# Kernel tuning notes

Measured on AMD Instinct MI355X. Metric: run time of the kernel, lower is better.

## Reference

```python
import jax, jax.numpy as jnp
import numpy as np

HEADS, DH = 8, 32

def _ln(x):
    m = x.mean(-1, keepdims=True)
    v = ((x - m) ** 2).mean(-1, keepdims=True)
    return (x - m) * jax.lax.rsqrt(v + 1e-5)

def _attn(xq, xk, ei, ea, wq, wk, wv, we, wo):
    # one relation: q from dst-type nodes xq, k/v from src-type nodes xk
    Nd, Ns, E = xq.shape[0], xk.shape[0], ea.shape[0]
    src, dst = ei[0], ei[1]
    q = (xq @ wq).reshape(Nd, HEADS, DH)
    k = (xk @ wk).reshape(Ns, HEADS, DH)
    v = (xk @ wv).reshape(Ns, HEADS, DH)
    e = (ea @ we).reshape(E, HEADS, DH)
    s = jnp.sum(q[dst] * (k[src] + e), axis=-1) * (DH ** -0.5)  # (E, heads)
    m = jax.ops.segment_max(s, dst, num_segments=Nd)
    m = jnp.where(jnp.isfinite(m), m, 0.0)
    ex = jnp.exp(s - m[dst])
    den = jax.ops.segment_sum(ex, dst, num_segments=Nd)
    msg = jax.ops.segment_sum(ex[:, :, None] * (v[src] + e), dst, num_segments=Nd)
    msg = msg / (den[:, :, None] + 1e-9)
    return msg.reshape(Nd, HEADS * DH) @ wo

def setup_inputs() -> dict:
    key = jax.random.key(0)
    ks = list(jax.random.split(key, 24))
    N, H, ED, L, F = 18432, 256, 64, 2, 512
    EA, ES = 294912, 65536
    nrm = lambda k, shp, s=1.0: jax.random.normal(k, shp, dtype=jnp.float32) * s
    inp = {}
    inp['all_feats_left'] = nrm(ks[0], (N, H))
    inp['all_feats_right'] = nrm(ks[1], (N, H))
    inp['ea_ll'] = nrm(ks[2], (EA, ED))
    inp['ea_rr'] = nrm(ks[3], (EA, ED))
    inp['ea_lr'] = nrm(ks[4], (ES, ED))
    inp['ea_rl'] = nrm(ks[5], (ES, ED))
    inp['ei_ll'] = jax.random.randint(ks[6], (2, EA), 0, N, dtype=jnp.int32)
    inp['ei_rr'] = jax.random.randint(ks[7], (2, EA), 0, N, dtype=jnp.int32)
    inp['ei_lr'] = jax.random.randint(ks[8], (2, ES), 0, N, dtype=jnp.int32)
    inp['ei_rl'] = jax.random.randint(ks[9], (2, ES), 0, N, dtype=jnp.int32)
    # relation order: 0=ll, 1=rr, 2=lr (src left -> dst right), 3=rl
    inp['Wq'] = nrm(ks[10], (L, 4, H, H), H ** -0.5)
    inp['Wk'] = nrm(ks[11], (L, 4, H, H), H ** -0.5)
    inp['Wv'] = nrm(ks[12], (L, 4, H, H), H ** -0.5)
    inp['We'] = nrm(ks[13], (L, 4, ED, H), ED ** -0.5)
    inp['Wo'] = nrm(ks[14], (L, 4, H, H), H ** -0.5)
    inp['ffn_w1'] = nrm(ks[15], (L, 2, H, F), H ** -0.5)
    inp['ffn_b1'] = jnp.zeros((L, 2, F), jnp.float32)
    inp['ffn_w2'] = nrm(ks[16], (L, 2, F, H), F ** -0.5)
    inp['ffn_b2'] = jnp.zeros((L, 2, H), jnp.float32)
    inp['head_w1'] = nrm(ks[17], (H, H), H ** -0.5)
    inp['head_b1'] = jnp.zeros((H,), jnp.float32)
    inp['head_w2'] = nrm(ks[18], (H, 7), H ** -0.5)
    inp['head_b2'] = jnp.zeros((7,), jnp.float32)
    inp['action_start'] = 2048  # slice(K, None), K current nodes per arm
    return inp

def reference(all_feats_left, all_feats_right, ea_ll, ea_rr, ea_lr, ea_rl,
              Wq, Wk, Wv, We, Wo, ffn_w1, ffn_b1, ffn_w2, ffn_b2,
              head_w1, head_b1, head_w2, head_b2,
              ei_ll, ei_rr, ei_lr, ei_rl, action_start):
    xl, xr = all_feats_left, all_feats_right
    L = Wq.shape[0]
    for l in range(L):
        agg_l = (_attn(xl, xl, ei_ll, ea_ll, Wq[l, 0], Wk[l, 0], Wv[l, 0], We[l, 0], Wo[l, 0])
                 + _attn(xl, xr, ei_rl, ea_rl, Wq[l, 3], Wk[l, 3], Wv[l, 3], We[l, 3], Wo[l, 3]))
        agg_r = (_attn(xr, xr, ei_rr, ea_rr, Wq[l, 1], Wk[l, 1], Wv[l, 1], We[l, 1], Wo[l, 1])
                 + _attn(xr, xl, ei_lr, ea_lr, Wq[l, 2], Wk[l, 2], Wv[l, 2], We[l, 2], Wo[l, 2]))
        xl = _ln(xl + agg_l)
        xr = _ln(xr + agg_r)
        xl = _ln(xl + jax.nn.gelu(xl @ ffn_w1[l, 0] + ffn_b1[l, 0]) @ ffn_w2[l, 0] + ffn_b2[l, 0])
        xr = _ln(xr + jax.nn.gelu(xr @ ffn_w1[l, 1] + ffn_b1[l, 1]) @ ffn_w2[l, 1] + ffn_b2[l, 1])
    la = xl[action_start:]
    ra = xr[action_start:]
    head = lambda z: jax.nn.gelu(z @ head_w1 + head_b1) @ head_w2 + head_b2
    return head(la), head(ra)
```

## Files before the change

### kernel.cpp

```cpp
#include <hip/hip_runtime.h>
#include <math.h>

typedef __attribute__((ext_vector_type(8))) short short8;
typedef __attribute__((ext_vector_type(4))) float f32x4;

__device__ __forceinline__ unsigned short f2bf(float f) {
  unsigned u = __builtin_bit_cast(unsigned, f);
  u += 0x7fff + ((u >> 16) & 1);
  return (unsigned short)(u >> 16);
}
__device__ __forceinline__ float bf2f(unsigned short h) {
  unsigned u = ((unsigned)h) << 16;
  return __builtin_bit_cast(float, u);
}
__device__ __forceinline__ float gelu_f(float x) {
  const float c0 = 0.7978845608028654f;
  return 0.5f * x * (1.0f + tanhf(c0 * (x + 0.044715f * x * x * x)));
}
__device__ __forceinline__ void gload16(const unsigned short* g, unsigned short* l) {
  __builtin_amdgcn_global_load_lds(
      (const __attribute__((address_space(1))) unsigned int*)g,
      (__attribute__((address_space(3))) unsigned int*)l, 16, 0, 0);
}

template<bool ACC, bool BIAS, bool GELU>
__global__ __launch_bounds__(256)
void gemm_mfma2_k(const unsigned short* __restrict__ A0, const unsigned short* __restrict__ A1,
                  int lda,
                  const unsigned short* __restrict__ BT0, const unsigned short* __restrict__ BT1,
                  const float* __restrict__ bias0, const float* __restrict__ bias1,
                  float* __restrict__ Cf0, float* __restrict__ Cf1, int Sf, int ldf,
                  unsigned short* __restrict__ Cb10, unsigned short* __restrict__ Cb11,
                  int S2, int ldb1,
                  unsigned short* __restrict__ Cb20, unsigned short* __restrict__ Cb21, int ldb2,
                  int M, int N, int K)
{
  const int z = blockIdx.z;
  const unsigned short* A  = z ? A1  : A0;
  const unsigned short* BT = z ? BT1 : BT0;
  const float* bias        = z ? bias1 : bias0;
  float* Cf                = z ? Cf1 : Cf0;
  unsigned short* Cb1      = z ? Cb11 : Cb10;
  unsigned short* Cb2      = z ? Cb21 : Cb20;

  __shared__ __align__(16) unsigned short As[128 * 32];
  __shared__ __align__(16) unsigned short Bs[128 * 32];
  const int tid = threadIdx.x;
  const int bm = blockIdx.x * 128, bn = blockIdx.y * 128;
  const int lane = tid & 63, w = tid >> 6;
  const int wr = w >> 1, wc = w & 1;
  const int l15 = lane & 15, kg = lane >> 4;

  const int srow0 = w * 16 + (lane >> 2);
  const int srow1 = 64 + srow0;
  const int sslot = lane & 3;
  const int koff0 = (((sslot - (srow0 >> 1)) & 3)) * 8;
  const int koff1 = (((sslot - (srow1 >> 1)) & 3)) * 8;
  const unsigned short* gA0 = A + (size_t)(bm + srow0) * lda + koff0;
  const unsigned short* gA1 = A + (size_t)(bm + srow1) * lda + koff1;
  const unsigned short* gB0 = BT + (size_t)(bn + srow0) * K + koff0;
  const unsigned short* gB1 = BT + (size_t)(bn + srow1) * K + koff1;
  unsigned short* lA0 = As + w * 512;
  unsigned short* lA1 = As + 2048 + w * 512;
  unsigned short* lB0 = Bs + w * 512;
  unsigned short* lB1 = Bs + 2048 + w * 512;

  f32x4 acc[4][4] = {};

  for (int k0 = 0; k0 < K; k0 += 32) {
    gload16(gA0 + k0, lA0);
    gload16(gA1 + k0, lA1);
    gload16(gB0 + k0, lB0);
    gload16(gB1 + k0, lB1);
    __syncthreads();
    short8 af[4], bfr[4];
#pragma unroll
    for (int m = 0; m < 4; ++m) {
      int row = wr * 64 + m * 16 + l15;
      int ph = (kg + (row >> 1)) & 3;
      af[m] = *(const short8*)(As + row * 32 + ph * 8);
    }
#pragma unroll
    for (int n = 0; n < 4; ++n) {
      int col = wc * 64 + n * 16 + l15;
      int ph = (kg + (col >> 1)) & 3;
      bfr[n] = *(const short8*)(Bs + col * 32 + ph * 8);
    }
#pragma unroll
    for (int m = 0; m < 4; ++m)
#pragma unroll
      for (int n = 0; n < 4; ++n)
        acc[m][n] = __builtin_amdgcn_mfma_f32_16x16x32_bf16(af[m], bfr[n], acc[m][n], 0, 0, 0);
    __syncthreads();
  }

#pragma unroll
  for (int m = 0; m < 4; ++m) {
#pragma unroll
    for (int n = 0; n < 4; ++n) {
      int col = bn + wc * 64 + n * 16 + l15;
      float bv = BIAS ? bias[col] : 0.f;
      f32x4 v = acc[m][n];
#pragma unroll
      for (int r2 = 0; r2 < 4; ++r2) {
        int row = bm + wr * 64 + m * 16 + kg * 4 + r2;
        float val = v[r2] + bv;
        if (GELU) val = gelu_f(val);
        if (col < Sf) {
          float* p = Cf + (size_t)row * ldf + col;
          if (ACC) val += *p;
          *p = val;
        } else if (col < S2) {
          Cb1[(size_t)row * ldb1 + (col - Sf)] = f2bf(val);
        } else {
          Cb2[(size_t)row * ldb2 + (col - S2)] = f2bf(val);
        }
      }
    }
  }
}

template<bool BIAS>
__global__ __launch_bounds__(256)
void gemm_k2(const float* __restrict__ A0, const float* __restrict__ A1,
             const float* __restrict__ B, const float* __restrict__ bias,
             float* __restrict__ C0, float* __restrict__ C1,
             int M, int N, int K)
{
  const float* A = blockIdx.z ? A1 : A0;
  float* C = blockIdx.z ? C1 : C0;
  __shared__ float As[16][132];
  __shared__ float Bs[16][132];
  const int tid = threadIdx.x;
  const int tx = tid & 15, ty = tid >> 4;
  const int bm = blockIdx.x * 128;
  float acc[8][8];
#pragma unroll
  for (int i = 0; i < 8; ++i)
#pragma unroll
    for (int j = 0; j < 8; ++j) acc[i][j] = 0.f;
  const int ar = tid >> 1;
  const int ac = (tid & 1) * 8;
  const int br = tid >> 4;
  const int bc = (tid & 15) * 8;
  for (int k0 = 0; k0 < K; k0 += 16) {
    {
      float av[8] = {0,0,0,0,0,0,0,0};
      if (bm + ar < M) {
        const float* app = A + (size_t)(bm + ar) * K + (k0 + ac);
        float4 a0 = *(const float4*)app;
        float4 a1 = *(const float4*)(app + 4);
        av[0]=a0.x; av[1]=a0.y; av[2]=a0.z; av[3]=a0.w;
        av[4]=a1.x; av[5]=a1.y; av[6]=a1.z; av[7]=a1.w;
      }
#pragma unroll
      for (int i = 0; i < 8; ++i) As[ac + i][ar] = av[i];
    }
    {
      float bv[8] = {0,0,0,0,0,0,0,0};
      const float* bpp = B + (size_t)(k0 + br) * N + bc;
#pragma unroll
      for (int i = 0; i < 8; ++i) { if (bc + i < N) bv[i] = bpp[i]; }
#pragma unroll
      for (int i = 0; i < 8; ++i) Bs[br][bc + i] = bv[i];
    }
    __syncthreads();
#pragma unroll
    for (int kk = 0; kk < 16; ++kk) {
      float a[8], b[8];
      float4 t0 = *(const float4*)&As[kk][ty * 8];
      float4 t1 = *(const float4*)&As[kk][ty * 8 + 4];
      float4 u0 = *(const float4*)&Bs[kk][tx * 8];
      float4 u1 = *(const float4*)&Bs[kk][tx * 8 + 4];
      a[0]=t0.x;a[1]=t0.y;a[2]=t0.z;a[3]=t0.w;a[4]=t1.x;a[5]=t1.y;a[6]=t1.z;a[7]=t1.w;
      b[0]=u0.x;b[1]=u0.y;b[2]=u0.z;b[3]=u0.w;b[4]=u1.x;b[5]=u1.y;b[6]=u1.z;b[7]=u1.w;
#pragma unroll
      for (int i = 0; i < 8; ++i)
#pragma unroll
        for (int j = 0; j < 8; ++j)
          acc[i][j] = fmaf(a[i], b[j], acc[i][j]);
    }
    __syncthreads();
  }
#pragma unroll
  for (int i = 0; i < 8; ++i) {
    int row = bm + ty * 8 + i;
    if (row >= M) continue;
    int colg = tx * 8;
    float* cp = C + (size_t)row * N + colg;
#pragma unroll
    for (int j = 0; j < 8; ++j) {
      int cc = colg + j;
      if (cc < N) {
        float val = acc[i][j];
        if (BIAS) val += bias[cc];
        cp[j] = val;
      }
    }
  }
}

__global__ void tc_k(const float* __restrict__ in, unsigned short* __restrict__ out,
                     int K, int N, int inStride, int outStride, int rowOff, int totK, int kOff)
{
  const int mat = blockIdx.y;
  const int idx = blockIdx.x * 256 + threadIdx.x;
  if (idx >= N * K) return;
  const int n = idx / K, k = idx - n * K;
  out[(size_t)mat * outStride + (size_t)(rowOff + n) * totK + kOff + k] =
      f2bf(in[(size_t)mat * inStride + (size_t)k * N + n]);
}

__global__ __launch_bounds__(256)
void wqe_k(unsigned short* __restrict__ BT, const float* __restrict__ We, int matStride)
{
  const int mat = blockIdx.y;
  const int oc = blockIdx.x;
  const int g = oc >> 6, cc = oc & 63;
  const int kin = threadIdx.x;
  const float* wrow = We + (size_t)mat * 16384 + (size_t)cc * 256 + g * 32;
  const unsigned short* bq = BT + (size_t)mat * matStride + (size_t)(g * 32) * 256 + kin;
  float acc = 0.f;
#pragma unroll 8
  for (int d = 0; d < 32; ++d)
    acc += bf2f(bq[(size_t)d * 256]) * wrow[d];
  BT[(size_t)mat * matStride + (size_t)(256 + oc) * 256 + kin] = f2bf(acc);
}

__global__ __launch_bounds__(256)
void wc_k(const float* __restrict__ We, const float* __restrict__ Wo,
          unsigned short* __restrict__ BTwo)
{
  const int mat = blockIdx.y;
  const int j = blockIdx.x;
  const int h = j >> 6, c = j & 63;
  const int n = threadIdx.x;
  const float* wep = We + (size_t)mat * 16384 + (size_t)c * 256 + h * 32;
  const float* wop = Wo + (size_t)mat * 65536 + (size_t)(h * 32) * 256 + n;
  float acc = 0.f;
#pragma unroll 8
  for (int d = 0; d < 32; ++d)
    acc += wep[d] * wop[(size_t)d * 256];
  BTwo[(size_t)mat * 196608 + (size_t)n * 768 + 256 + j] = f2bf(acc);
}

template<bool EABF>
__global__ __launch_bounds__(256)
void edge_attn_k(const int* __restrict__ offs, const int2* __restrict__ pairs,
                 const void* __restrict__ eaP, unsigned short* qTmsg,
                 const unsigned short* __restrict__ kv, int Nn)
{
  const int wv = (blockIdx.x * blockDim.x + threadIdx.x) >> 6;
  if (wv >= Nn) return;
  const int lane = threadIdx.x & 63;
  const int g = lane >> 3, p = lane & 7;
  const float scale = 0.17677669529663687f;
  const ushort4 qu = *(const ushort4*)(qTmsg + (size_t)wv * 768 + lane * 4);
  const float qx = bf2f(qu.x), qy = bf2f(qu.y), qz = bf2f(qu.z), qw = bf2f(qu.w);
  const unsigned short* Tp = qTmsg + (size_t)wv * 768 + 256 + g * 64 + p * 8;
  const ushort4 tu0 = *(const ushort4*)Tp;
  const ushort4 tu1 = *(const ushort4*)(Tp + 4);
  const float Ta0 = bf2f(tu0.x), Ta1 = bf2f(tu0.y), Ta2 = bf2f(tu0.z), Ta3 = bf2f(tu0.w);
  const float Tc0 = bf2f(tu1.x), Tc1 = bf2f(tu1.y), Tc2 = bf2f(tu1.z), Tc3 = bf2f(tu1.w);
  float m = -INFINITY, den = 0.f;
  float ax = 0.f, ay = 0.f, az = 0.f, aw = 0.f;
  float G[8] = {0,0,0,0,0,0,0,0};
  const int e0 = __builtin_amdgcn_readfirstlane(offs[wv]);
  const int e1 = __builtin_amdgcn_readfirstlane(offs[wv + 1]);
  for (int j = e0; j < e1; j += 2) {
    const bool hasB = (j + 1) < e1;
    const int2 prA = pairs[j];
    const int2 prB = hasB ? pairs[j + 1] : prA;
    float eA[8], eB[8];
    if (EABF) {
      const unsigned short* ebp = (const unsigned short*)eaP;
      const short8 eAu = *(const short8*)(ebp + (size_t)prA.x * 64 + p * 8);
      const short8 eBu = *(const short8*)(ebp + (size_t)prB.x * 64 + p * 8);
#pragma unroll
      for (int i = 0; i < 8; ++i) {
        eA[i] = bf2f((unsigned short)eAu[i]);
        eB[i] = bf2f((unsigned short)eBu[i]);
      }
    } else {
      const float* efp = (const float*)eaP;
      const float4 a0 = *(const float4*)(efp + (size_t)prA.x * 64 + p * 8);
      const float4 a1 = *(const float4*)(efp + (size_t)prA.x * 64 + p * 8 + 4);
      const float4 b0 = *(const float4*)(efp + (size_t)prB.x * 64 + p * 8);
      const float4 b1 = *(const float4*)(efp + (size_t)prB.x * 64 + p * 8 + 4);
      eA[0]=a0.x; eA[1]=a0.y; eA[2]=a0.z; eA[3]=a0.w;
      eA[4]=a1.x; eA[5]=a1.y; eA[6]=a1.z; eA[7]=a1.w;
      eB[0]=b0.x; eB[1]=b0.y; eB[2]=b0.z; eB[3]=b0.w;
      eB[4]=b1.x; eB[5]=b1.y; eB[6]=b1.z; eB[7]=b1.w;
    }
    const unsigned short* kpA = kv + (size_t)prA.y * 512 + lane * 4;
    const unsigned short* kpB = kv + (size_t)prB.y * 512 + lane * 4;
    const ushort4 kAu = *(const ushort4*)kpA;
    const ushort4 vAu = *(const ushort4*)(kpA + 256);
    const ushort4 kBu = *(const ushort4*)kpB;
    const ushort4 vBu = *(const ushort4*)(kpB + 256);
    float pA = qx * bf2f(kAu.x) + qy * bf2f(kAu.y) + qz * bf2f(kAu.z) + qw * bf2f(kAu.w);
    pA += eA[0]*Ta0 + eA[1]*Ta1 + eA[2]*Ta2 + eA[3]*Ta3;
    pA += eA[4]*Tc0 + eA[5]*Tc1 + eA[6]*Tc2 + eA[7]*Tc3;
    float pB = qx * bf2f(kBu.x) + qy * bf2f(kBu.y) + qz * bf2f(kBu.z) + qw * bf2f(kBu.w);
    pB += eB[0]*Ta0 + eB[1]*Ta1 + eB[2]*Ta2 + eB[3]*Ta3;
    pB += eB[4]*Tc0 + eB[5]*Tc1 + eB[6]*Tc2 + eB[7]*Tc3;
    pA += __shfl_xor(pA, 1, 64); pA += __shfl_xor(pA, 2, 64); pA += __shfl_xor(pA, 4, 64);
    pB += __shfl_xor(pB, 1, 64); pB += __shfl_xor(pB, 2, 64); pB += __shfl_xor(pB, 4, 64);
    const float sA = pA * scale;
    const float sB = hasB ? pB * scale : -INFINITY;
    const float mn = fmaxf(m, fmaxf(sA, sB));
    const float corr = __expf(m - mn);
    const float wA = __expf(sA - mn);
    const float wB = __expf(sB - mn);
    m = mn;
    den = den * corr + wA + wB;
    ax = ax * corr + wA * bf2f(vAu.x) + wB * bf2f(vBu.x);
    ay = ay * corr + wA * bf2f(vAu.y) + wB * bf2f(vBu.y);
    az = az * corr + wA * bf2f(vAu.z) + wB * bf2f(vBu.z);
    aw = aw * corr + wA * bf2f(vAu.w) + wB * bf2f(vBu.w);
#pragma unroll
    for (int i = 0; i < 8; ++i)
      G[i] = G[i] * corr + wA * eA[i] + wB * eB[i];
  }
  const float inv = 1.f / (den + 1e-9f);
  ushort4 o;
  o.x = f2bf(ax * inv); o.y = f2bf(ay * inv);
  o.z = f2bf(az * inv); o.w = f2bf(aw * inv);
  *(ushort4*)(qTmsg + (size_t)wv * 768 + lane * 4) = o;
  short8 gn;
#pragma unroll
  for (int i = 0; i < 8; ++i) gn[i] = (short)f2bf(G[i] * inv);
  *(short8*)(qTmsg + (size_t)wv * 768 + 256 + g * 64 + p * 8) = gn;
}

__global__ __launch_bounds__(256)
void add_ln2_k(unsigned short* __restrict__ xbL, const float* __restrict__ addL,
               unsigned short* __restrict__ xbR, const float* __restrict__ addR, int Nn)
{
  unsigned short* xb = blockIdx.y ? xbR : xbL;
  const float* add = blockIdx.y ? addR : addL;
  const int wv = (blockIdx.x * blockDim.x + threadIdx.x) >> 6;
  if (wv >= Nn) return;
  const int lane = threadIdx.x & 63;
  ushort4 xu = *(const ushort4*)(xb + (size_t)wv * 256 + lane * 4);
  float4 av = *(const float4*)(add + (size_t)wv * 256 + lane * 4);
  float4 y;
  y.x = bf2f(xu.x) + av.x; y.y = bf2f(xu.y) + av.y;
  y.z = bf2f(xu.z) + av.z; y.w = bf2f(xu.w) + av.w;
  float s = y.x + y.y + y.z + y.w;
#pragma unroll
  for (int msk = 1; msk < 64; msk <<= 1) s += __shfl_xor(s, msk, 64);
  const float mean = s * (1.f / 256.f);
  float4 d;
  d.x = y.x - mean; d.y = y.y - mean; d.z = y.z - mean; d.w = y.w - mean;
  float sq = d.x*d.x + d.y*d.y + d.z*d.z + d.w*d.w;
#pragma unroll
  for (int msk = 1; msk < 64; msk <<= 1) sq += __shfl_xor(sq, msk, 64);
  const float r = rsqrtf(sq * (1.f / 256.f) + 1e-5f);
  ushort4 ob;
  ob.x = f2bf(d.x * r); ob.y = f2bf(d.y * r);
  ob.z = f2bf(d.z * r); ob.w = f2bf(d.w * r);
  *(ushort4*)(xb + (size_t)wv * 256 + lane * 4) = ob;
}

__global__ void cvt_x2_k(const float* __restrict__ aL, unsigned short* __restrict__ xbL,
                         const float* __restrict__ aR, unsigned short* __restrict__ xbR, int n4)
{
  const float* a = blockIdx.y ? aR : aL;
  unsigned short* xb = blockIdx.y ? xbR : xbL;
  int i = blockIdx.x * 256 + threadIdx.x;
  if (i >= n4) return;
  float4 v = ((const float4*)a)[i];
  ushort4 b;
  b.x = f2bf(v.x); b.y = f2bf(v.y); b.z = f2bf(v.z); b.w = f2bf(v.w);
  ((ushort4*)xb)[i] = b;
}

__global__ void cvt_ea2_k(const float* __restrict__ s0, const float* __restrict__ s1,
                          unsigned short* __restrict__ d0, unsigned short* __restrict__ d1,
                          int n8a, int n8b)
{
  const float* src = blockIdx.y ? s1 : s0;
  unsigned short* dst = blockIdx.y ? d1 : d0;
  const int n8 = blockIdx.y ? n8b : n8a;
  int i = blockIdx.x * 256 + threadIdx.x;
  if (i >= n8) return;
  float4 a = ((const float4*)src)[i * 2];
  float4 b = ((const float4*)src)[i * 2 + 1];
  short8 o;
  o[0] = (short)f2bf(a.x); o[1] = (short)f2bf(a.y);
  o[2] = (short)f2bf(a.z); o[3] = (short)f2bf(a.w);
  o[4] = (short)f2bf(b.x); o[5] = (short)f2bf(b.y);
  o[6] = (short)f2bf(b.z); o[7] = (short)f2bf(b.w);
  *(short8*)(dst + (size_t)i * 8) = o;
}

__global__ void zero4_k(int* p, int n) {
  int i = blockIdx.x * 256 + threadIdx.x;
  if (i < n) p[i] = 0;
}
__global__ void hist4_k(const int* d0, const int* d1, const int* d2, const int* d3,
                        int E0, int E1, int E2, int E3, int* cnt, int Nn) {
  const int s = blockIdx.y;
  const int* d = (s == 0) ? d0 : (s == 1) ? d1 : (s == 2) ? d2 : d3;
  const int E = (s == 0) ? E0 : (s == 1) ? E1 : (s == 2) ? E2 : E3;
  int e = blockIdx.x * 256 + threadIdx.x;
  if (e < E) atomicAdd(&cnt[s * Nn + d[e]], 1);
}
__global__ __launch_bounds__(256)
void scan4_k(const int* __restrict__ cnt, int* __restrict__ offs, int* __restrict__ cursor, int Nn)
{
  __shared__ int sums[256];
  const int s = blockIdx.x;
  const int t = threadIdx.x;
  const int* c = cnt + (size_t)s * Nn;
  int* o = offs + (size_t)s * (Nn + 1);
  int* cur = cursor + (size_t)s * Nn;
  const int chunk = (Nn + 255) / 256;
  const int base = t * chunk;
  int sl = 0;
  for (int i = 0; i < chunk; ++i) {
    int idx = base + i;
    if (idx < Nn) sl += c[idx];
  }
  sums[t] = sl;
  __syncthreads();
  for (int off = 1; off < 256; off <<= 1) {
    int val = (t >= off) ? sums[t - off] : 0;
    __syncthreads();
    sums[t] += val;
    __syncthreads();
  }
  int run = (t == 0) ? 0 : sums[t - 1];
  for (int i = 0; i < chunk; ++i) {
    int idx = base + i;
    if (idx < Nn) { o[idx] = run; cur[idx] = run; run += c[idx]; }
  }
  if (t == 255) o[Nn] = run;
}
__global__ void scatter4_k(const int* e0p, const int* e1p, const int* e2p, const int* e3p,
                           int E0, int E1, int E2, int E3, int* cursor,
                           int2* p0, int2* p1, int2* p2, int2* p3, int Nn) {
  const int s = blockIdx.y;
  const int* ei = (s == 0) ? e0p : (s == 1) ? e1p : (s == 2) ? e2p : e3p;
  int2* po = (s == 0) ? p0 : (s == 1) ? p1 : (s == 2) ? p2 : p3;
  const int E = (s == 0) ? E0 : (s == 1) ? E1 : (s == 2) ? E2 : E3;
  int e = blockIdx.x * 256 + threadIdx.x;
  if (e < E) {
    int pos = atomicAdd(&cursor[s * Nn + ei[E + e]], 1);
    po[pos] = make_int2(e, ei[e]);
  }
}

extern "C" void kernel_launch(void* const* d_in, const int* in_sizes, int n_in,
                              void* d_out, int out_size, void* d_ws, size_t ws_size,
                              hipStream_t stream)
{
  (void)n_in; (void)ws_size;
  const float* afl = (const float*)d_in[0];
  const float* afr = (const float*)d_in[1];
  const float* eaA[4] = {(const float*)d_in[2], (const float*)d_in[3],
                         (const float*)d_in[4], (const float*)d_in[5]};
  const int* eiA[4] = {(const int*)d_in[6], (const int*)d_in[7],
                       (const int*)d_in[8], (const int*)d_in[9]};
  const float* Wq  = (const float*)d_in[10];
  const float* Wk  = (const float*)d_in[11];
  const float* Wv  = (const float*)d_in[12];
  const float* We  = (const float*)d_in[13];
  const float* Wo  = (const float*)d_in[14];
  const float* fw1 = (const float*)d_in[15];
  const float* fb1 = (const float*)d_in[16];
  const float* fw2 = (const float*)d_in[17];
  const float* fb2 = (const float*)d_in[18];
  const float* hw1 = (const float*)d_in[19];
  const float* hb1 = (const float*)d_in[20];
  const float* hw2 = (const float*)d_in[21];
  const float* hb2 = (const float*)d_in[22];

  const int Nn = in_sizes[0] / 256;
  const int E[4] = {in_sizes[2] / 64, in_sizes[3] / 64, in_sizes[4] / 64, in_sizes[5] / 64};
  const int Mh = out_size / 14;
  const int astart = Nn - Mh;
  float* out = (float*)d_out;

  char* wsp = (char*)d_ws;
  auto alloc = [&](size_t bytes) -> void* {
    void* pp = (void*)wsp;
    wsp += (bytes + 255) & ~(size_t)255;
    return pp;
  };
  unsigned short* xlb = (unsigned short*)alloc((size_t)Nn * 256 * 2);
  unsigned short* xrb = (unsigned short*)alloc((size_t)Nn * 256 * 2);
  float* aggL = (float*)alloc((size_t)Nn * 256 * 4);
  float* aggR = (float*)alloc((size_t)Nn * 256 * 4);
  unsigned short* qTbA = (unsigned short*)alloc((size_t)Nn * 768 * 2);
  unsigned short* qTbB = (unsigned short*)alloc((size_t)Nn * 768 * 2);
  unsigned short* kvbA = (unsigned short*)alloc((size_t)Nn * 512 * 2);
  unsigned short* kvbB = (unsigned short*)alloc((size_t)Nn * 512 * 2);
  unsigned short* BTqkvT = (unsigned short*)alloc((size_t)8 * 1280 * 256 * 2);
  unsigned short* BTwo   = (unsigned short*)alloc((size_t)8 * 256 * 768 * 2);
  unsigned short* BTf1   = (unsigned short*)alloc((size_t)4 * 512 * 256 * 2);
  unsigned short* BTf2   = (unsigned short*)alloc((size_t)4 * 256 * 512 * 2);
  unsigned short* BTh1   = (unsigned short*)alloc((size_t)256 * 256 * 2);
  unsigned short* eabf0  = (unsigned short*)alloc((size_t)E[0] * 64 * 2);
  unsigned short* eabf1  = (unsigned short*)alloc((size_t)E[1] * 64 * 2);
  int* offs4 = (int*)alloc((size_t)4 * (Nn + 1) * 4);
  int* cnt4  = (int*)alloc((size_t)4 * Nn * 4);
  int* cur4  = (int*)alloc((size_t)4 * Nn * 4);
  int2* pairs[4];
  for (int s = 0; s < 4; ++s) pairs[s] = (int2*)alloc((size_t)E[s] * 8);

  const dim3 B256(256);
  const int wgNodes = (Nn * 64 + 255) / 256;
  int maxE = E[0];
  for (int s = 1; s < 4; ++s) if (E[s] > maxE) maxE = E[s];

  cvt_x2_k<<<dim3((Nn * 64 + 255) / 256, 2), B256, 0, stream>>>(afl, xlb, afr, xrb, Nn * 64);
  {
    int n8a = E[0] * 8, n8b = E[1] * 8;
    int gx = ((n8a > n8b ? n8a : n8b) + 255) / 256;
    cvt_ea2_k<<<dim3(gx, 2), B256, 0, stream>>>(eaA[0], eaA[1], eabf0, eabf1, n8a, n8b);
  }
  zero4_k<<<dim3((4 * Nn + 255) / 256), B256, 0, stream>>>(cnt4, 4 * Nn);
  {
    dim3 gh((maxE + 255) / 256, 4);
    hist4_k<<<gh, B256, 0, stream>>>(eiA[0] + E[0], eiA[1] + E[1], eiA[2] + E[2], eiA[3] + E[3],
                                     E[0], E[1], E[2], E[3], cnt4, Nn);
    scan4_k<<<dim3(4), B256, 0, stream>>>(cnt4, offs4, cur4, Nn);
    scatter4_k<<<gh, B256, 0, stream>>>(eiA[0], eiA[1], eiA[2], eiA[3],
                                        E[0], E[1], E[2], E[3], cur4,
                                        pairs[0], pairs[1], pairs[2], pairs[3], Nn);
  }
  {
    dim3 g8((65536 + 255) / 256, 8);
    tc_k<<<g8, B256, 0, stream>>>(Wq, BTqkvT, 256, 256, 65536, 327680, 0,    256, 0);
    tc_k<<<g8, B256, 0, stream>>>(Wk, BTqkvT, 256, 256, 65536, 327680, 768,  256, 0);
    tc_k<<<g8, B256, 0, stream>>>(Wv, BTqkvT, 256, 256, 65536, 327680, 1024, 256, 0);
    wqe_k<<<dim3(512, 8), B256, 0, stream>>>(BTqkvT, We, 327680);
    tc_k<<<g8, B256, 0, stream>>>(Wo, BTwo, 256, 256, 65536, 196608, 0, 768, 0);
    wc_k<<<dim3(512, 8), B256, 0, stream>>>(We, Wo, BTwo);
    tc_k<<<dim3((131072 + 255) / 256, 4), B256, 0, stream>>>(fw1, BTf1, 256, 512, 131072, 131072, 0, 256, 0);
    tc_k<<<dim3((131072 + 255) / 256, 4), B256, 0, stream>>>(fw2, BTf2, 512, 256, 131072, 131072, 0, 512, 0);
    tc_k<<<dim3((65536 + 255) / 256, 1), B256, 0, stream>>>(hw1, BTh1, 256, 256, 0, 0, 0, 256, 0);
  }

  auto mfma2 = [&](const unsigned short* A0, const unsigned short* A1, int lda,
                   const unsigned short* BT0, const unsigned short* BT1,
                   const float* bias0, const float* bias1,
                   float* Cf0, float* Cf1, int Sf, int ldf,
                   unsigned short* Cb10, unsigned short* Cb11, int S2, int ldb1,
                   unsigned short* Cb20, unsigned short* Cb21, int ldb2,
                   int M, int N, int K, bool accf, bool biasf, bool gelu) {
    dim3 g(M / 128, N / 128, 2);
    if (accf)
      gemm_mfma2_k<true, false, false><<<g, B256, 0, stream>>>(A0, A1, lda, BT0, BT1, bias0, bias1,
          Cf0, Cf1, Sf, ldf, Cb10, Cb11, S2, ldb1, Cb20, Cb21, ldb2, M, N, K);
    else if (biasf && gelu)
      gemm_mfma2_k<false, true, true ><<<g, B256, 0, stream>>>(A0, A1, lda, BT0, BT1, bias0, bias1,
          Cf0, Cf1, Sf, ldf, Cb10, Cb11, S2, ldb1, Cb20, Cb21, ldb2, M, N, K);
    else if (biasf)
      gemm_mfma2_k<false, true, false><<<g, B256, 0, stream>>>(A0, A1, lda, BT0, BT1, bias0, bias1,
          Cf0, Cf1, Sf, ldf, Cb10, Cb11, S2, ldb1, Cb20, Cb21, ldb2, M, N, K);
    else
      gemm_mfma2_k<false, false, false><<<g, B256, 0, stream>>>(A0, A1, lda, BT0, BT1, bias0, bias1,
          Cf0, Cf1, Sf, ldf, Cb10, Cb11, S2, ldb1, Cb20, Cb21, ldb2, M, N, K);
  };
  auto edge = [&](int s, unsigned short* qTmsg, const unsigned short* kvb) {
    if (s <= 1) {
      const unsigned short* eb = s == 0 ? eabf0 : eabf1;
      edge_attn_k<true><<<dim3(wgNodes), B256, 0, stream>>>(
          offs4 + (size_t)s * (Nn + 1), pairs[s], (const void*)eb, qTmsg, kvb, Nn);
    } else {
      edge_attn_k<false><<<dim3(wgNodes), B256, 0, stream>>>(
          offs4 + (size_t)s * (Nn + 1), pairs[s], (const void*)eaA[s], qTmsg, kvb, Nn);
    }
  };

  for (int l = 0; l < 2; ++l) {
    const unsigned short* btLL = BTqkvT + (size_t)(l*4+0) * 327680;
    const unsigned short* btRR = BTqkvT + (size_t)(l*4+1) * 327680;
    const unsigned short* btLR = BTqkvT + (size_t)(l*4+2) * 327680;
    const unsigned short* btRL = BTqkvT + (size_t)(l*4+3) * 327680;
    mfma2(xlb, xrb, 256, btLL, btRR, nullptr, nullptr, nullptr, nullptr, 0, 0,
          qTbA, qTbB, 768, 768, kvbA, kvbB, 512, Nn, 1280, 256, false, false, false);
    edge(0, qTbA, kvbA);
    edge(1, qTbB, kvbB);
    mfma2(qTbA, qTbB, 768, BTwo + (size_t)(l*4+0)*196608, BTwo + (size_t)(l*4+1)*196608,
          nullptr, nullptr, aggL, aggR, 256, 256, nullptr, nullptr, 0, 0, nullptr, nullptr, 0,
          Nn, 256, 768, false, false, false);
    mfma2(xlb, xrb, 256, btRL, btLR, nullptr, nullptr, nullptr, nullptr, 0, 0,
          qTbA, qTbB, 768, 768, nullptr, nullptr, 0, Nn, 768, 256, false, false, false);
    mfma2(xrb, xlb, 256, btRL + (size_t)768 * 256, btLR + (size_t)768 * 256,
          nullptr, nullptr, nullptr, nullptr, 0, 0,
          nullptr, nullptr, 0, 0, kvbA, kvbB, 512, Nn, 512, 256, false, false, false);
    edge(3, qTbA, kvbA);
    edge(2, qTbB, kvbB);
    mfma2(qTbA, qTbB, 768, BTwo + (size_t)(l*4+3)*196608, BTwo + (size_t)(l*4+2)*196608,
          nullptr, nullptr, aggL, aggR, 256, 256, nullptr, nullptr, 0, 0, nullptr, nullptr, 0,
          Nn, 256, 768, true, false, false);
    add_ln2_k<<<dim3(wgNodes, 2), B256, 0, stream>>>(xlb, aggL, xrb, aggR, Nn);
    const int fL = l * 2 + 0, fR = l * 2 + 1;
    mfma2(xlb, xrb, 256, BTf1 + (size_t)fL*131072, BTf1 + (size_t)fR*131072,
          fb1 + (size_t)fL*512, fb1 + (size_t)fR*512, nullptr, nullptr, 0, 0,
          nullptr, nullptr, 0, 0, kvbA, kvbB, 512, Nn, 512, 256, false, true, true);
    mfma2(kvbA, kvbB, 512, BTf2 + (size_t)fL*131072, BTf2 + (size_t)fR*131072,
          fb2 + (size_t)fL*256, fb2 + (size_t)fR*256, aggL, aggR, 256, 256,
          nullptr, nullptr, 0, 0, nullptr, nullptr, 0, Nn, 256, 512, false, true, false);
    add_ln2_k<<<dim3(wgNodes, 2), B256, 0, stream>>>(xlb, aggL, xrb, aggR, Nn);
  }
  mfma2(xlb + (size_t)astart * 256, xrb + (size_t)astart * 256, 256, BTh1, BTh1,
        hb1, hb1, aggL, aggR, 256, 256, nullptr, nullptr, 0, 0, nullptr, nullptr, 0,
        Mh, 256, 256, false, true, true);
  gemm_k2<true><<<dim3(Mh / 128, 1, 2), B256, 0, stream>>>(aggL, aggR, hw2, hb2,
                                                           out, out + (size_t)Mh * 7, Mh, 7, 256);
}
```

Before: 1.256 ms.

## Batch cross-relation projections and fuse both relations' output projections into one GEMM

```diff
diff --git a/kernel.cpp b/kernel.cpp
--- a/kernel.cpp
+++ b/kernel.cpp
@@ -23,7 +23,7 @@
       (__attribute__((address_space(3))) unsigned int*)l, 16, 0, 0);
 }
 
-template<bool ACC, bool BIAS, bool GELU>
+template<bool BIAS, bool GELU>
 __global__ __launch_bounds__(256)
 void gemm_mfma2_k(const unsigned short* __restrict__ A0, const unsigned short* __restrict__ A1,
                   int lda,
@@ -65,6 +65,18 @@
   unsigned short* lB0 = Bs + w * 512;
   unsigned short* lB1 = Bs + 2048 + w * 512;
 
+  int roffA[4], roffB[4];
+#pragma unroll
+  for (int m = 0; m < 4; ++m) {
+    int row = wr * 64 + m * 16 + l15;
+    roffA[m] = row * 32 + ((kg + (row >> 1)) & 3) * 8;
+  }
+#pragma unroll
+  for (int n = 0; n < 4; ++n) {
+    int col = wc * 64 + n * 16 + l15;
+    roffB[n] = col * 32 + ((kg + (col >> 1)) & 3) * 8;
+  }
+
   f32x4 acc[4][4] = {};
 
   for (int k0 = 0; k0 < K; k0 += 32) {
@@ -75,17 +87,9 @@
     __syncthreads();
     short8 af[4], bfr[4];
 #pragma unroll
-    for (int m = 0; m < 4; ++m) {
-      int row = wr * 64 + m * 16 + l15;
-      int ph = (kg + (row >> 1)) & 3;
-      af[m] = *(const short8*)(As + row * 32 + ph * 8);
-    }
-#pragma unroll
-    for (int n = 0; n < 4; ++n) {
-      int col = wc * 64 + n * 16 + l15;
-      int ph = (kg + (col >> 1)) & 3;
-      bfr[n] = *(const short8*)(Bs + col * 32 + ph * 8);
-    }
+    for (int m = 0; m < 4; ++m) af[m] = *(const short8*)(As + roffA[m]);
+#pragma unroll
+    for (int n = 0; n < 4; ++n) bfr[n] = *(const short8*)(Bs + roffB[n]);
 #pragma unroll
     for (int m = 0; m < 4; ++m)
 #pragma unroll
@@ -107,14 +111,97 @@
         float val = v[r2] + bv;
         if (GELU) val = gelu_f(val);
         if (col < Sf) {
-          float* p = Cf + (size_t)row * ldf + col;
-          if (ACC) val += *p;
-          *p = val;
+          Cf[(size_t)row * ldf + col] = val;
         } else if (col < S2) {
           Cb1[(size_t)row * ldb1 + (col - Sf)] = f2bf(val);
         } else {
           Cb2[(size_t)row * ldb2 + (col - S2)] = f2bf(val);
         }
+      }
+    }
+  }
+}
+
+__global__ __launch_bounds__(256)
+void gemm_mfma4_k(const unsigned short* __restrict__ Ax0, const unsigned short* __restrict__ Ax1,
+                  const unsigned short* __restrict__ Ax2, const unsigned short* __restrict__ Ax3,
+                  const unsigned short* __restrict__ Bx0, const unsigned short* __restrict__ Bx1,
+                  const unsigned short* __restrict__ Bx2, const unsigned short* __restrict__ Bx3,
+                  unsigned short* __restrict__ Cx0, unsigned short* __restrict__ Cx1,
+                  unsigned short* __restrict__ Cx2, unsigned short* __restrict__ Cx3,
+                  int ldb01, int ldb23, int N01, int N23, int lda, int K, int M)
+{
+  const int z = blockIdx.z;
+  const unsigned short* A; const unsigned short* BT; unsigned short* C;
+  int ldb, Nz;
+  if (z == 0)      { A = Ax0; BT = Bx0; C = Cx0; ldb = ldb01; Nz = N01; }
+  else if (z == 1) { A = Ax1; BT = Bx1; C = Cx1; ldb = ldb01; Nz = N01; }
+  else if (z == 2) { A = Ax2; BT = Bx2; C = Cx2; ldb = ldb23; Nz = N23; }
+  else             { A = Ax3; BT = Bx3; C = Cx3; ldb = ldb23; Nz = N23; }
+  const int bm = blockIdx.x * 128, bn = blockIdx.y * 128;
+  if (bn >= Nz) return;
+
+  __shared__ __align__(16) unsigned short As[128 * 32];
+  __shared__ __align__(16) unsigned short Bs[128 * 32];
+  const int tid = threadIdx.x;
+  const int lane = tid & 63, w = tid >> 6;
+  const int wr = w >> 1, wc = w & 1;
+  const int l15 = lane & 15, kg = lane >> 4;
+  const int srow0 = w * 16 + (lane >> 2);
+  const int srow1 = 64 + srow0;
+  const int sslot = lane & 3;
+  const int koff0 = (((sslot - (srow0 >> 1)) & 3)) * 8;
+  const int koff1 = (((sslot - (srow1 >> 1)) & 3)) * 8;
+  const unsigned short* gA0 = A + (size_t)(bm + srow0) * lda + koff0;
+  const unsigned short* gA1 = A + (size_t)(bm + srow1) * lda + koff1;
+  const unsigned short* gB0 = BT + (size_t)(bn + srow0) * K + koff0;
+  const unsigned short* gB1 = BT + (size_t)(bn + srow1) * K + koff1;
+  unsigned short* lA0 = As + w * 512;
+  unsigned short* lA1 = As + 2048 + w * 512;
+  unsigned short* lB0 = Bs + w * 512;
+  unsigned short* lB1 = Bs + 2048 + w * 512;
+
+  int roffA[4], roffB[4];
+#pragma unroll
+  for (int m = 0; m < 4; ++m) {
+    int row = wr * 64 + m * 16 + l15;
+    roffA[m] = row * 32 + ((kg + (row >> 1)) & 3) * 8;
+  }
+#pragma unroll
+  for (int n = 0; n < 4; ++n) {
+    int col = wc * 64 + n * 16 + l15;
+    roffB[n] = col * 32 + ((kg + (col >> 1)) & 3) * 8;
+  }
+
+  f32x4 acc[4][4] = {};
+  for (int k0 = 0; k0 < K; k0 += 32) {
+    gload16(gA0 + k0, lA0);
+    gload16(gA1 + k0, lA1);
+    gload16(gB0 + k0, lB0);
+    gload16(gB1 + k0, lB1);
+    __syncthreads();
+    short8 af[4], bfr[4];
+#pragma unroll
+    for (int m = 0; m < 4; ++m) af[m] = *(const short8*)(As + roffA[m]);
+#pragma unroll
+    for (int n = 0; n < 4; ++n) bfr[n] = *(const short8*)(Bs + roffB[n]);
+#pragma unroll
+    for (int m = 0; m < 4; ++m)
+#pragma unroll
+      for (int n = 0; n < 4; ++n)
+        acc[m][n] = __builtin_amdgcn_mfma_f32_16x16x32_bf16(af[m], bfr[n], acc[m][n], 0, 0, 0);
+    __syncthreads();
+  }
+#pragma unroll
+  for (int m = 0; m < 4; ++m) {
+#pragma unroll
+    for (int n = 0; n < 4; ++n) {
+      int col = bn + wc * 64 + n * 16 + l15;
+      f32x4 v = acc[m][n];
+#pragma unroll
+      for (int r2 = 0; r2 < 4; ++r2) {
+        int row = bm + wr * 64 + m * 16 + kg * 4 + r2;
+        C[(size_t)row * ldb + col] = f2bf(v[r2]);
       }
     }
   }
@@ -211,6 +298,19 @@
       f2bf(in[(size_t)mat * inStride + (size_t)k * N + n]);
 }
 
+__global__ void tc_qkv_k(const float* __restrict__ Wq, const float* __restrict__ Wk,
+                         const float* __restrict__ Wv, unsigned short* __restrict__ out)
+{
+  const int zz = blockIdx.z;
+  const float* in = (zz == 0) ? Wq : (zz == 1) ? Wk : Wv;
+  const int rowOff = (zz == 0) ? 0 : (zz == 1) ? 768 : 1024;
+  const int mat = blockIdx.y;
+  const int idx = blockIdx.x * 256 + threadIdx.x;
+  const int n = idx >> 8, k = idx & 255;
+  out[(size_t)mat * 327680 + (size_t)(rowOff + n) * 256 + k] =
+      f2bf(in[(size_t)mat * 65536 + (size_t)k * 256 + n]);
+}
+
 __global__ __launch_bounds__(256)
 void wqe_k(unsigned short* __restrict__ BT, const float* __restrict__ We, int matStride)
 {
@@ -227,9 +327,21 @@
   BT[(size_t)mat * matStride + (size_t)(256 + oc) * 256 + kin] = f2bf(acc);
 }
 
+__global__ void wo_tc_k(const float* __restrict__ Wo, unsigned short* __restrict__ BTwoF)
+{
+  const int mat = blockIdx.y;
+  const int idx = blockIdx.x * 256 + threadIdx.x;
+  const int n = idx >> 8, k = idx & 255;
+  const int l = mat >> 2, i = mat & 3;
+  const int side = (i == 1 || i == 2) ? 1 : 0;
+  const int base = (i >= 2) ? 768 : 0;
+  BTwoF[(size_t)(l * 2 + side) * 393216 + (size_t)n * 1536 + base + k] =
+      f2bf(Wo[(size_t)mat * 65536 + (size_t)k * 256 + n]);
+}
+
 __global__ __launch_bounds__(256)
 void wc_k(const float* __restrict__ We, const float* __restrict__ Wo,
-          unsigned short* __restrict__ BTwo)
+          unsigned short* __restrict__ BTwoF)
 {
   const int mat = blockIdx.y;
   const int j = blockIdx.x;
@@ -241,23 +353,35 @@
 #pragma unroll 8
   for (int d = 0; d < 32; ++d)
     acc += wep[d] * wop[(size_t)d * 256];
-  BTwo[(size_t)mat * 196608 + (size_t)n * 768 + 256 + j] = f2bf(acc);
+  const int l = mat >> 2, i = mat & 3;
+  const int side = (i == 1 || i == 2) ? 1 : 0;
+  const int base = (i >= 2) ? 768 : 0;
+  BTwoF[(size_t)(l * 2 + side) * 393216 + (size_t)n * 1536 + base + 256 + j] = f2bf(acc);
 }
 
 template<bool EABF>
 __global__ __launch_bounds__(256)
-void edge_attn_k(const int* __restrict__ offs, const int2* __restrict__ pairs,
-                 const void* __restrict__ eaP, unsigned short* qTmsg,
-                 const unsigned short* __restrict__ kv, int Nn)
-{
+void edge2_k(const int* __restrict__ o0, const int* __restrict__ o1,
+             const int2* __restrict__ p0, const int2* __restrict__ p1,
+             const void* __restrict__ e0, const void* __restrict__ e1,
+             unsigned short* q0, unsigned short* q1,
+             const unsigned short* __restrict__ k0, const unsigned short* __restrict__ k1,
+             int Nn)
+{
+  const int y = blockIdx.y;
+  const int* offs = y ? o1 : o0;
+  const int2* pairs = y ? p1 : p0;
+  const void* eaP = y ? e1 : e0;
+  unsigned short* qTmsg = y ? q1 : q0;
+  const unsigned short* kv = y ? k1 : k0;
   const int wv = (blockIdx.x * blockDim.x + threadIdx.x) >> 6;
   if (wv >= Nn) return;
   const int lane = threadIdx.x & 63;
   const int g = lane >> 3, p = lane & 7;
   const float scale = 0.17677669529663687f;
-  const ushort4 qu = *(const ushort4*)(qTmsg + (size_t)wv * 768 + lane * 4);
+  const ushort4 qu = *(const ushort4*)(qTmsg + (size_t)wv * 1536 + lane * 4);
   const float qx = bf2f(qu.x), qy = bf2f(qu.y), qz = bf2f(qu.z), qw = bf2f(qu.w);
-  const unsigned short* Tp = qTmsg + (size_t)wv * 768 + 256 + g * 64 + p * 8;
+  const unsigned short* Tp = qTmsg + (size_t)wv * 1536 + 256 + g * 64 + p * 8;
   const ushort4 tu0 = *(const ushort4*)Tp;
   const ushort4 tu1 = *(const ushort4*)(Tp + 4);
   const float Ta0 = bf2f(tu0.x), Ta1 = bf2f(tu0.y), Ta2 = bf2f(tu0.z), Ta3 = bf2f(tu0.w);
@@ -265,10 +389,10 @@
   float m = -INFINITY, den = 0.f;
   float ax = 0.f, ay = 0.f, az = 0.f, aw = 0.f;
   float G[8] = {0,0,0,0,0,0,0,0};
-  const int e0 = __builtin_amdgcn_readfirstlane(offs[wv]);
-  const int e1 = __builtin_amdgcn_readfirstlane(offs[wv + 1]);
-  for (int j = e0; j < e1; j += 2) {
-    const bool hasB = (j + 1) < e1;
+  const int e0i = __builtin_amdgcn_readfirstlane(offs[wv]);
+  const int e1i = __builtin_amdgcn_readfirstlane(offs[wv + 1]);
+  for (int j = e0i; j < e1i; j += 2) {
+    const bool hasB = (j + 1) < e1i;
     const int2 prA = pairs[j];
     const int2 prB = hasB ? pairs[j + 1] : prA;
     float eA[8], eB[8];
@@ -326,27 +450,27 @@
   ushort4 o;
   o.x = f2bf(ax * inv); o.y = f2bf(ay * inv);
   o.z = f2bf(az * inv); o.w = f2bf(aw * inv);
-  *(ushort4*)(qTmsg + (size_t)wv * 768 + lane * 4) = o;
+  *(ushort4*)(qTmsg + (size_t)wv * 1536 + lane * 4) = o;
   short8 gn;
 #pragma unroll
   for (int i = 0; i < 8; ++i) gn[i] = (short)f2bf(G[i] * inv);
-  *(short8*)(qTmsg + (size_t)wv * 768 + 256 + g * 64 + p * 8) = gn;
+  *(short8*)(qTmsg + (size_t)wv * 1536 + 256 + g * 64 + p * 8) = gn;
 }
 
 __global__ __launch_bounds__(256)
-void add_ln2_k(unsigned short* __restrict__ xbL, const float* __restrict__ addL,
-               unsigned short* __restrict__ xbR, const float* __restrict__ addR, int Nn)
+void add_ln2_k(unsigned short* __restrict__ xbL, const unsigned short* __restrict__ addL,
+               unsigned short* __restrict__ xbR, const unsigned short* __restrict__ addR, int Nn)
 {
   unsigned short* xb = blockIdx.y ? xbR : xbL;
-  const float* add = blockIdx.y ? addR : addL;
+  const unsigned short* add = blockIdx.y ? addR : addL;
   const int wv = (blockIdx.x * blockDim.x + threadIdx.x) >> 6;
   if (wv >= Nn) return;
   const int lane = threadIdx.x & 63;
   ushort4 xu = *(const ushort4*)(xb + (size_t)wv * 256 + lane * 4);
-  float4 av = *(const float4*)(add + (size_t)wv * 256 + lane * 4);
+  ushort4 au = *(const ushort4*)(add + (size_t)wv * 256 + lane * 4);
   float4 y;
-  y.x = bf2f(xu.x) + av.x; y.y = bf2f(xu.y) + av.y;
-  y.z = bf2f(xu.z) + av.z; y.w = bf2f(xu.w) + av.w;
+  y.x = bf2f(xu.x) + bf2f(au.x); y.y = bf2f(xu.y) + bf2f(au.y);
+  y.z = bf2f(xu.z) + bf2f(au.z); y.w = bf2f(xu.w) + bf2f(au.w);
   float s = y.x + y.y + y.z + y.w;
 #pragma unroll
   for (int msk = 1; msk < 64; msk <<= 1) s += __shfl_xor(s, msk, 64);
@@ -376,13 +500,8 @@
   ((ushort4*)xb)[i] = b;
 }
 
-__global__ void cvt_ea2_k(const float* __restrict__ s0, const float* __restrict__ s1,
-                          unsigned short* __restrict__ d0, unsigned short* __restrict__ d1,
-                          int n8a, int n8b)
-{
-  const float* src = blockIdx.y ? s1 : s0;
-  unsigned short* dst = blockIdx.y ? d1 : d0;
-  const int n8 = blockIdx.y ? n8b : n8a;
+__global__ void cvt_ea1_k(const float* __restrict__ src, unsigned short* __restrict__ dst, int n8)
+{
   int i = blockIdx.x * 256 + threadIdx.x;
   if (i >= n8) return;
   float4 a = ((const float4*)src)[i * 2];
@@ -491,19 +610,18 @@
   };
   unsigned short* xlb = (unsigned short*)alloc((size_t)Nn * 256 * 2);
   unsigned short* xrb = (unsigned short*)alloc((size_t)Nn * 256 * 2);
-  float* aggL = (float*)alloc((size_t)Nn * 256 * 4);
-  float* aggR = (float*)alloc((size_t)Nn * 256 * 4);
-  unsigned short* qTbA = (unsigned short*)alloc((size_t)Nn * 768 * 2);
-  unsigned short* qTbB = (unsigned short*)alloc((size_t)Nn * 768 * 2);
+  unsigned short* aggLb = (unsigned short*)alloc((size_t)Nn * 256 * 2);
+  unsigned short* aggRb = (unsigned short*)alloc((size_t)Nn * 256 * 2);
+  unsigned short* qTmsgA = (unsigned short*)alloc((size_t)Nn * 1536 * 2);
+  unsigned short* qTmsgB = (unsigned short*)alloc((size_t)Nn * 1536 * 2);
   unsigned short* kvbA = (unsigned short*)alloc((size_t)Nn * 512 * 2);
   unsigned short* kvbB = (unsigned short*)alloc((size_t)Nn * 512 * 2);
   unsigned short* BTqkvT = (unsigned short*)alloc((size_t)8 * 1280 * 256 * 2);
-  unsigned short* BTwo   = (unsigned short*)alloc((size_t)8 * 256 * 768 * 2);
+  unsigned short* BTwoF  = (unsigned short*)alloc((size_t)4 * 256 * 1536 * 2);
   unsigned short* BTf1   = (unsigned short*)alloc((size_t)4 * 512 * 256 * 2);
   unsigned short* BTf2   = (unsigned short*)alloc((size_t)4 * 256 * 512 * 2);
   unsigned short* BTh1   = (unsigned short*)alloc((size_t)256 * 256 * 2);
   unsigned short* eabf0  = (unsigned short*)alloc((size_t)E[0] * 64 * 2);
-  unsigned short* eabf1  = (unsigned short*)alloc((size_t)E[1] * 64 * 2);
   int* offs4 = (int*)alloc((size_t)4 * (Nn + 1) * 4);
   int* cnt4  = (int*)alloc((size_t)4 * Nn * 4);
   int* cur4  = (int*)alloc((size_t)4 * Nn * 4);
@@ -516,11 +634,7 @@
   for (int s = 1; s < 4; ++s) if (E[s] > maxE) maxE = E[s];
 
   cvt_x2_k<<<dim3((Nn * 64 + 255) / 256, 2), B256, 0, stream>>>(afl, xlb, afr, xrb, Nn * 64);
-  {
-    int n8a = E[0] * 8, n8b = E[1] * 8;
-    int gx = ((n8a > n8b ? n8a : n8b) + 255) / 256;
-    cvt_ea2_k<<<dim3(gx, 2), B256, 0, stream>>>(eaA[0], eaA[1], eabf0, eabf1, n8a, n8b);
-  }
+  cvt_ea1_k<<<dim3((E[0] * 8 + 255) / 256), B256, 0, stream>>>(eaA[0], eabf0, E[0] * 8);
   zero4_k<<<dim3((4 * Nn + 255) / 256), B256, 0, stream>>>(cnt4, 4 * Nn);
   {
     dim3 gh((maxE + 255) / 256, 4);
@@ -532,13 +646,10 @@
                                         pairs[0], pairs[1], pairs[2], pairs[3], Nn);
   }
   {
-    dim3 g8((65536 + 255) / 256, 8);
-    tc_k<<<g8, B256, 0, stream>>>(Wq, BTqkvT, 256, 256, 65536, 327680, 0,    256, 0);
-    tc_k<<<g8, B256, 0, stream>>>(Wk, BTqkvT, 256, 256, 65536, 327680, 768,  256, 0);
-    tc_k<<<g8, B256, 0, stream>>>(Wv, BTqkvT, 256, 256, 65536, 327680, 1024, 256, 0);
+    tc_qkv_k<<<dim3(256, 8, 3), B256, 0, stream>>>(Wq, Wk, Wv, BTqkvT);
     wqe_k<<<dim3(512, 8), B256, 0, stream>>>(BTqkvT, We, 327680);
-    tc_k<<<g8, B256, 0, stream>>>(Wo, BTwo, 256, 256, 65536, 196608, 0, 768, 0);
-    wc_k<<<dim3(512, 8), B256, 0, stream>>>(We, Wo, BTwo);
+    wo_tc_k<<<dim3(256, 8), B256, 0, stream>>>(Wo, BTwoF);
+    wc_k<<<dim3(512, 8), B256, 0, stream>>>(We, Wo, BTwoF);
     tc_k<<<dim3((131072 + 255) / 256, 4), B256, 0, stream>>>(fw1, BTf1, 256, 512, 131072, 131072, 0, 256, 0);
     tc_k<<<dim3((131072 + 255) / 256, 4), B256, 0, stream>>>(fw2, BTf2, 512, 256, 131072, 131072, 0, 512, 0);
     tc_k<<<dim3((65536 + 255) / 256, 1), B256, 0, stream>>>(hw1, BTh1, 256, 256, 0, 0, 0, 256, 0);
@@ -550,30 +661,17 @@
                    float* Cf0, float* Cf1, int Sf, int ldf,
                    unsigned short* Cb10, unsigned short* Cb11, int S2, int ldb1,
                    unsigned short* Cb20, unsigned short* Cb21, int ldb2,
-                   int M, int N, int K, bool accf, bool biasf, bool gelu) {
+                   int M, int N, int K, bool biasf, bool gelu) {
     dim3 g(M / 128, N / 128, 2);
-    if (accf)
-      gemm_mfma2_k<true, false, false><<<g, B256, 0, stream>>>(A0, A1, lda, BT0, BT1, bias0, bias1,
-          Cf0, Cf1, Sf, ldf, Cb10, Cb11, S2, ldb1, Cb20, Cb21, ldb2, M, N, K);
-    else if (biasf && gelu)
-      gemm_mfma2_k<false, true, true ><<<g, B256, 0, stream>>>(A0, A1, lda, BT0, BT1, bias0, bias1,
+    if (biasf && gelu)
+      gemm_mfma2_k<true, true ><<<g, B256, 0, stream>>>(A0, A1, lda, BT0, BT1, bias0, bias1,
           Cf0, Cf1, Sf, ldf, Cb10, Cb11, S2, ldb1, Cb20, Cb21, ldb2, M, N, K);
     else if (biasf)
-      gemm_mfma2_k<false, true, false><<<g, B256, 0, stream>>>(A0, A1, lda, BT0, BT1, bias0, bias1,
+      gemm_mfma2_k<true, false><<<g, B256, 0, stream>>>(A0, A1, lda, BT0, BT1, bias0, bias1,
           Cf0, Cf1, Sf, ldf, Cb10, Cb11, S2, ldb1, Cb20, Cb21, ldb2, M, N, K);
     else
-      gemm_mfma2_k<false, false, false><<<g, B256, 0, stream>>>(A0, A1, lda, BT0, BT1, bias0, bias1,
+      gemm_mfma2_k<false, false><<<g, B256, 0, stream>>>(A0, A1, lda, BT0, BT1, bias0, bias1,
           Cf0, Cf1, Sf, ldf, Cb10, Cb11, S2, ldb1, Cb20, Cb21, ldb2, M, N, K);
-  };
-  auto edge = [&](int s, unsigned short* qTmsg, const unsigned short* kvb) {
-    if (s <= 1) {
-      const unsigned short* eb = s == 0 ? eabf0 : eabf1;
-      edge_attn_k<true><<<dim3(wgNodes), B256, 0, stream>>>(
-          offs4 + (size_t)s * (Nn + 1), pairs[s], (const void*)eb, qTmsg, kvb, Nn);
-    } else {
-      edge_attn_k<false><<<dim3(wgNodes), B256, 0, stream>>>(
-          offs4 + (size_t)s * (Nn + 1), pairs[s], (const void*)eaA[s], qTmsg, kvb, Nn);
-    }
   };
 
   for (int l = 0; l < 2; ++l) {
@@ -582,35 +680,38 @@
     const unsigned short* btLR = BTqkvT + (size_t)(l*4+2) * 327680;
     const unsigned short* btRL = BTqkvT + (size_t)(l*4+3) * 327680;
     mfma2(xlb, xrb, 256, btLL, btRR, nullptr, nullptr, nullptr, nullptr, 0, 0,
-          qTbA, qTbB, 768, 768, kvbA, kvbB, 512, Nn, 1280, 256, false, false, false);
-    edge(0, qTbA, kvbA);
-    edge(1, qTbB, kvbB);
-    mfma2(qTbA, qTbB, 768, BTwo + (size_t)(l*4+0)*196608, BTwo + (size_t)(l*4+1)*196608,
-          nullptr, nullptr, aggL, aggR, 256, 256, nullptr, nullptr, 0, 0, nullptr, nullptr, 0,
-          Nn, 256, 768, false, false, false);
-    mfma2(xlb, xrb, 256, btRL, btLR, nullptr, nullptr, nullptr, nullptr, 0, 0,
-          qTbA, qTbB, 768, 768, nullptr, nullptr, 0, Nn, 768, 256, false, false, false);
-    mfma2(xrb, xlb, 256, btRL + (size_t)768 * 256, btLR + (size_t)768 * 256,
-          nullptr, nullptr, nullptr, nullptr, 0, 0,
-          nullptr, nullptr, 0, 0, kvbA, kvbB, 512, Nn, 512, 256, false, false, false);
-    edge(3, qTbA, kvbA);
-    edge(2, qTbB, kvbB);
-    mfma2(qTbA, qTbB, 768, BTwo + (size_t)(l*4+3)*196608, BTwo + (size_t)(l*4+2)*196608,
-          nullptr, nullptr, aggL, aggR, 256, 256, nullptr, nullptr, 0, 0, nullptr, nullptr, 0,
-          Nn, 256, 768, true, false, false);
-    add_ln2_k<<<dim3(wgNodes, 2), B256, 0, stream>>>(xlb, aggL, xrb, aggR, Nn);
+          qTmsgA, qTmsgB, 768, 1536, kvbA, kvbB, 512, Nn, 1280, 256, false, false);
+    edge2_k<true><<<dim3(wgNodes, 1), B256, 0, stream>>>(
+        offs4, offs4, pairs[0], pairs[0], eabf0, eabf0, qTmsgA, qTmsgA, kvbA, kvbA, Nn);
+    edge2_k<false><<<dim3(wgNodes, 1), B256, 0, stream>>>(
+        offs4 + (size_t)(Nn + 1), offs4 + (size_t)(Nn + 1), pairs[1], pairs[1],
+        eaA[1], eaA[1], qTmsgB, qTmsgB, kvbB, kvbB, Nn);
+    gemm_mfma4_k<<<dim3(Nn / 128, 6, 4), B256, 0, stream>>>(
+        xlb, xrb, xrb, xlb,
+        btRL, btLR, btRL + (size_t)768 * 256, btLR + (size_t)768 * 256,
+        qTmsgA + 768, qTmsgB + 768, kvbA, kvbB,
+        1536, 512, 768, 512, 256, 256, Nn);
+    edge2_k<false><<<dim3(wgNodes, 2), B256, 0, stream>>>(
+        offs4 + (size_t)3 * (Nn + 1), offs4 + (size_t)2 * (Nn + 1), pairs[3], pairs[2],
+        eaA[3], eaA[2], qTmsgA + 768, qTmsgB + 768, kvbA, kvbB, Nn);
+    mfma2(qTmsgA, qTmsgB, 1536, BTwoF + (size_t)(l*2+0)*393216, BTwoF + (size_t)(l*2+1)*393216,
+          nullptr, nullptr, nullptr, nullptr, 0, 0, aggLb, aggRb, 256, 256,
+          nullptr, nullptr, 0, Nn, 256, 1536, false, false);
+    add_ln2_k<<<dim3(wgNodes, 2), B256, 0, stream>>>(xlb, aggLb, xrb, aggRb, Nn);
     const int fL = l * 2 + 0, fR = l * 2 + 1;
     mfma2(xlb, xrb, 256, BTf1 + (size_t)fL*131072, BTf1 + (size_t)fR*131072,
           fb1 + (size_t)fL*512, fb1 + (size_t)fR*512, nullptr, nullptr, 0, 0,
-          nullptr, nullptr, 0, 0, kvbA, kvbB, 512, Nn, 512, 256, false, true, true);
+          nullptr, nullptr, 0, 0, kvbA, kvbB, 512, Nn, 512, 256, true, true);
     mfma2(kvbA, kvbB, 512, BTf2 + (size_t)fL*131072, BTf2 + (size_t)fR*131072,
-          fb2 + (size_t)fL*256, fb2 + (size_t)fR*256, aggL, aggR, 256, 256,
-          nullptr, nullptr, 0, 0, nullptr, nullptr, 0, Nn, 256, 512, false, true, false);
-    add_ln2_k<<<dim3(wgNodes, 2), B256, 0, stream>>>(xlb, aggL, xrb, aggR, Nn);
-  }
+          fb2 + (size_t)fL*256, fb2 + (size_t)fR*256, nullptr, nullptr, 0, 0,
+          aggLb, aggRb, 256, 256, nullptr, nullptr, 0, Nn, 256, 512, true, false);
+    add_ln2_k<<<dim3(wgNodes, 2), B256, 0, stream>>>(xlb, aggLb, xrb, aggRb, Nn);
+  }
+  float* h1L = (float*)kvbA;
+  float* h1R = (float*)kvbB;
   mfma2(xlb + (size_t)astart * 256, xrb + (size_t)astart * 256, 256, BTh1, BTh1,
-        hb1, hb1, aggL, aggR, 256, 256, nullptr, nullptr, 0, 0, nullptr, nullptr, 0,
-        Mh, 256, 256, false, true, true);
-  gemm_k2<true><<<dim3(Mh / 128, 1, 2), B256, 0, stream>>>(aggL, aggR, hw2, hb2,
+        hb1, hb1, h1L, h1R, 256, 256, nullptr, nullptr, 0, 0, nullptr, nullptr, 0,
+        Mh, 256, 256, true, true);
+  gemm_k2<true><<<dim3(Mh / 128, 1, 2), B256, 0, stream>>>(h1L, h1R, hw2, hb2,
                                                            out, out + (size_t)Mh * 7, Mh, 7, 256);
 }
```

Result: faster. 1.162 ms (-7.5%).
